# Optimization experiments

Hardware: AMD Instinct MI355X
Metric: run time of the kernel (lower is better)

## Reference

```python
import jax, jax.numpy as jnp
import numpy as np

V_W_MAX = 2.2
H = 16777216


def setup_inputs() -> dict:
    key = jax.random.key(0)
    k0, k1 = jax.random.split(key)
    x0 = jax.random.normal(k0, (4,), dtype=jnp.float32)
    U = jax.random.normal(k1, (H, 2), dtype=jnp.float32)
    dt = jnp.float32(0.05)
    return {"x0": x0, "U": U, "dt": dt}


def reference(x0, U, dt):
    # The torch loop has recurrence only in x,y (a running sum); vx,vy depend
    # solely on U[t], so the whole trajectory is elementwise + cumsum.
    vmax = jnp.float32(V_W_MAX)
    uv = jnp.tanh(U) * vmax                       # [H,2] = (vx, vy)
    pos = x0[:2] + jnp.cumsum(uv * dt, axis=0)    # [H,2] integrated x,y
    theta = jnp.arctan2(uv[:, 1], uv[:, 0] + 1e-9)            # [H]
    v = jnp.clip(jnp.sqrt(uv[:, 0] * uv[:, 0] + uv[:, 1] * uv[:, 1] + 1e-12),
                 0.0, vmax)                                    # [H]
    rest = jnp.concatenate([pos, theta[:, None], v[:, None]], axis=1)  # [H,4]
    return jnp.concatenate([x0[None, :], rest], axis=0)       # [H+1,4]
```

## Files before the change

kernel.cpp:

```cpp
#include <hip/hip_runtime.h>

#define B1 256
#define IT1 8
#define CH1 (B1 * IT1)
#define B3 256
#define IT3 8
#define CH3 (B3 * IT3)
#define B2 1024
#define VMAX 2.2f

typedef float f32x4 __attribute__((ext_vector_type(4)));

struct DSum { double x, y; };

__device__ __forceinline__ float fast_tanh(float x) {
  float e = __expf(2.0f * x);
  return 1.0f - 2.0f / (e + 1.0f);
}

__device__ __forceinline__ float fast_atan2(float y, float x) {
  float ax = fabsf(x), ay = fabsf(y);
  float mn = fminf(ax, ay), mx = fmaxf(ax, ay);
  float a = mn / (mx + 1e-30f);
  float s = a * a;
  float r = ((-0.0464964749f * s + 0.15931422f) * s - 0.327622764f) * s * a + a;
  if (ay > ax) r = 1.57079637f - r;
  if (x < 0.0f) r = 3.14159274f - r;
  return copysignf(r, y);
}

__global__ __launch_bounds__(B1) void wi_partial(
    const float* __restrict__ U, const float* __restrict__ dtp,
    DSum* __restrict__ bsum, int N)
{
  const int t = threadIdx.x;
  const int lane = t & 63, wid = t >> 6;
  const long base = (long)blockIdx.x * CH1 + (long)t * IT1;
  float sx = 0.f, sy = 0.f;
  if (base + IT1 <= (long)N) {
    const f32x4* p = (const f32x4*)(U + 2 * base);
    #pragma unroll
    for (int i = 0; i < IT1 / 2; ++i) {
      f32x4 a = p[i];
      sx += fast_tanh(a.x) + fast_tanh(a.z);
      sy += fast_tanh(a.y) + fast_tanh(a.w);
    }
  } else {
    for (int i = 0; i < IT1; ++i) {
      long idx = base + i;
      if (idx < N) { sx += fast_tanh(U[2*idx]); sy += fast_tanh(U[2*idx+1]); }
    }
  }
  #pragma unroll
  for (int o = 1; o < 64; o <<= 1) { sx += __shfl_xor(sx, o); sy += __shfl_xor(sy, o); }
  __shared__ double wsx[B1/64], wsy[B1/64];
  if (lane == 0) { wsx[wid] = (double)sx; wsy[wid] = (double)sy; }
  __syncthreads();
  if (t == 0) {
    const float sc = VMAX * (*dtp);
    double ax = 0.0, ay = 0.0;
    #pragma unroll
    for (int w = 0; w < B1/64; ++w) { ax += wsx[w]; ay += wsy[w]; }
    bsum[blockIdx.x].x = ax * (double)sc;
    bsum[blockIdx.x].y = ay * (double)sc;
  }
}

__global__ __launch_bounds__(B2) void wi_scan_blocks(DSum* bsum, int nblocks)
{
  const int t = threadIdx.x;
  const int lane = t & 63, wid = t >> 6;
  const int per = (nblocks + B2 - 1) / B2;
  const int s = t * per;
  const int e = min(s + per, nblocks);
  double tx = 0.0, ty = 0.0;
  for (int i = s; i < e; ++i) { tx += bsum[i].x; ty += bsum[i].y; }
  double ix = tx, iy = ty;
  #pragma unroll
  for (int o = 1; o < 64; o <<= 1) {
    double ux = __shfl_up(ix, o);
    double uy = __shfl_up(iy, o);
    if (lane >= o) { ix += ux; iy += uy; }
  }
  __shared__ double wx[B2/64], wy[B2/64];
  if (lane == 63) { wx[wid] = ix; wy[wid] = iy; }
  __syncthreads();
  double wbx = 0.0, wby = 0.0;
  #pragma unroll
  for (int w = 0; w < B2/64; ++w) {
    if (w < wid) { wbx += wx[w]; wby += wy[w]; }
  }
  double rx = wbx + ix - tx;
  double ry = wby + iy - ty;
  for (int i = s; i < e; ++i) {
    double vx = bsum[i].x, vy = bsum[i].y;
    bsum[i].x = rx; bsum[i].y = ry;
    rx += vx; ry += vy;
  }
}

__global__ __launch_bounds__(B3) void wi_emit(
    const float* __restrict__ U, const float* __restrict__ x0,
    const float* __restrict__ dtp, const DSum* __restrict__ boff,
    float* __restrict__ out, int N)
{
  __shared__ f32x4 stage[CH3];
  __shared__ float wsum_x[B3/64], wsum_y[B3/64];

  const int t = threadIdx.x;
  const int lane = t & 63, wid = t >> 6;
  const long base = (long)blockIdx.x * CH3 + (long)t * IT3;
  const float dt = *dtp;

  float vx[IT3], vy[IT3];
  const bool full = (base + IT3 <= (long)N);
  if (full) {
    const f32x4* p = (const f32x4*)(U + 2 * base);
    #pragma unroll
    for (int i = 0; i < IT3 / 2; ++i) {
      f32x4 a = p[i];
      vx[2*i]   = fast_tanh(a.x) * VMAX; vy[2*i]   = fast_tanh(a.y) * VMAX;
      vx[2*i+1] = fast_tanh(a.z) * VMAX; vy[2*i+1] = fast_tanh(a.w) * VMAX;
    }
  } else {
    for (int i = 0; i < IT3; ++i) {
      long idx = base + i;
      if (idx < N) { vx[i] = fast_tanh(U[2*idx]) * VMAX; vy[i] = fast_tanh(U[2*idx+1]) * VMAX; }
      else { vx[i] = 0.f; vy[i] = 0.f; }
    }
  }

  float px[IT3], py[IT3];
  float sx = 0.f, sy = 0.f;
  #pragma unroll
  for (int i = 0; i < IT3; ++i) { sx += vx[i]*dt; px[i] = sx; sy += vy[i]*dt; py[i] = sy; }
  const float totx = sx, toty = sy;

  #pragma unroll
  for (int o = 1; o < 64; o <<= 1) {
    float ux = __shfl_up(sx, o);
    float uy = __shfl_up(sy, o);
    if (lane >= o) { sx += ux; sy += uy; }
  }
  if (lane == 63) { wsum_x[wid] = sx; wsum_y[wid] = sy; }
  __syncthreads();
  float wbx = 0.f, wby = 0.f;
  #pragma unroll
  for (int w = 0; w < B3/64; ++w) {
    if (w < wid) { wbx += wsum_x[w]; wby += wsum_y[w]; }
  }
  const float exb = wbx + sx - totx;
  const float eyb = wby + sy - toty;

  const double ox = boff[blockIdx.x].x + (double)x0[0];
  const double oy = boff[blockIdx.x].y + (double)x0[1];

  #pragma unroll
  for (int i = 0; i < IT3; ++i) {
    float posx = (float)(ox + (double)(exb + px[i]));
    float posy = (float)(oy + (double)(eyb + py[i]));
    float th = fast_atan2(vy[i], vx[i] + 1e-9f);
    float vv = fminf(sqrtf(vx[i]*vx[i] + vy[i]*vy[i] + 1e-12f), VMAX);
    f32x4 r; r.x = posx; r.y = posy; r.z = th; r.w = vv;
    const int k = t * IT3 + i;
    stage[k ^ ((k >> 3) & 7)] = r;
  }
  __syncthreads();

  const long tile0 = (long)blockIdx.x * CH3;
  f32x4* o4 = (f32x4*)out;
  #pragma unroll
  for (int i = 0; i < IT3; ++i) {
    const int k = i * B3 + t;
    const long g = tile0 + k;
    if (g < (long)N) __builtin_nontemporal_store(stage[k ^ ((k >> 3) & 7)], o4 + 1 + g);
  }
  if (blockIdx.x == 0 && t == 0) {
    f32x4 r; r.x = x0[0]; r.y = x0[1]; r.z = x0[2]; r.w = x0[3];
    o4[0] = r;
  }
}

extern "C" void kernel_launch(void* const* d_in, const int* in_sizes, int n_in,
                              void* d_out, int out_size, void* d_ws, size_t ws_size,
                              hipStream_t stream) {
  const float* x0 = (const float*)d_in[0];
  const float* U  = (const float*)d_in[1];
  const float* dt = (const float*)d_in[2];
  float* out = (float*)d_out;
  const int N = in_sizes[1] / 2;
  const int nb1 = (N + CH1 - 1) / CH1;
  const int nb3 = (N + CH3 - 1) / CH3;
  DSum* bsum = (DSum*)d_ws;

  wi_partial<<<nb1, B1, 0, stream>>>(U, dt, bsum, N);
  wi_scan_blocks<<<1, B2, 0, stream>>>(bsum, nb1);
  wi_emit<<<nb3, B3, 0, stream>>>(U, x0, dt, bsum, out, N);
}
```

Measured before the change: 108.5 us.

## Use strided element mapping in emit kernel to drop LDS staging transpose

The emit kernel now assigns elements to threads with stride B3, so loads and output stores are directly coalesced. The shared-memory staging buffer and the per-thread serial prefix are gone. In their place, each of the 8 rows gets its own wave-level shuffle scan, combined through small per-row shared arrays. This removes the LDS round trip and one barrier, but costs 8 times more shuffle-scan work and narrower 8-byte loads.

```diff
diff --git a/kernel.cpp b/kernel.cpp
--- a/kernel.cpp
+++ b/kernel.cpp
@@ -10,6 +10,7 @@
 #define VMAX 2.2f
 
 typedef float f32x4 __attribute__((ext_vector_type(4)));
+typedef float f32x2 __attribute__((ext_vector_type(2)));
 
 struct DSum { double x, y; };
 
@@ -104,80 +105,74 @@
     const float* __restrict__ dtp, const DSum* __restrict__ boff,
     float* __restrict__ out, int N)
 {
-  __shared__ f32x4 stage[CH3];
-  __shared__ float wsum_x[B3/64], wsum_y[B3/64];
-
   const int t = threadIdx.x;
   const int lane = t & 63, wid = t >> 6;
-  const long base = (long)blockIdx.x * CH3 + (long)t * IT3;
+  const long tile0 = (long)blockIdx.x * CH3;
   const float dt = *dtp;
 
-  float vx[IT3], vy[IT3];
-  const bool full = (base + IT3 <= (long)N);
-  if (full) {
-    const f32x4* p = (const f32x4*)(U + 2 * base);
+  float uvx[IT3], uvy[IT3];
+  #pragma unroll
+  for (int r = 0; r < IT3; ++r) {
+    const long idx = tile0 + (long)r * B3 + t;
+    f32x2 a;
+    if (idx < (long)N) a = *(const f32x2*)(U + 2 * idx);
+    else { a.x = 0.f; a.y = 0.f; }
+    uvx[r] = fast_tanh(a.x) * VMAX;
+    uvy[r] = fast_tanh(a.y) * VMAX;
+  }
+
+  float isx[IT3], isy[IT3];
+  #pragma unroll
+  for (int r = 0; r < IT3; ++r) { isx[r] = uvx[r] * dt; isy[r] = uvy[r] * dt; }
+  #pragma unroll
+  for (int o = 1; o < 64; o <<= 1) {
     #pragma unroll
-    for (int i = 0; i < IT3 / 2; ++i) {
-      f32x4 a = p[i];
-      vx[2*i]   = fast_tanh(a.x) * VMAX; vy[2*i]   = fast_tanh(a.y) * VMAX;
-      vx[2*i+1] = fast_tanh(a.z) * VMAX; vy[2*i+1] = fast_tanh(a.w) * VMAX;
-    }
-  } else {
-    for (int i = 0; i < IT3; ++i) {
-      long idx = base + i;
-      if (idx < N) { vx[i] = fast_tanh(U[2*idx]) * VMAX; vy[i] = fast_tanh(U[2*idx+1]) * VMAX; }
-      else { vx[i] = 0.f; vy[i] = 0.f; }
+    for (int r = 0; r < IT3; ++r) {
+      float ux = __shfl_up(isx[r], o);
+      float uy = __shfl_up(isy[r], o);
+      if (lane >= o) { isx[r] += ux; isy[r] += uy; }
     }
   }
 
-  float px[IT3], py[IT3];
-  float sx = 0.f, sy = 0.f;
+  __shared__ float wtx[IT3][B3/64], wty[IT3][B3/64];
+  if (lane == 63) {
+    #pragma unroll
+    for (int r = 0; r < IT3; ++r) { wtx[r][wid] = isx[r]; wty[r][wid] = isy[r]; }
+  }
+  __syncthreads();
+  float offx[IT3], offy[IT3];
+  float rax = 0.f, ray = 0.f;
   #pragma unroll
-  for (int i = 0; i < IT3; ++i) { sx += vx[i]*dt; px[i] = sx; sy += vy[i]*dt; py[i] = sy; }
-  const float totx = sx, toty = sy;
-
-  #pragma unroll
-  for (int o = 1; o < 64; o <<= 1) {
-    float ux = __shfl_up(sx, o);
-    float uy = __shfl_up(sy, o);
-    if (lane >= o) { sx += ux; sy += uy; }
+  for (int r = 0; r < IT3; ++r) {
+    float wox = 0.f, woy = 0.f, rtx = 0.f, rty = 0.f;
+    #pragma unroll
+    for (int w = 0; w < B3/64; ++w) {
+      float a = wtx[r][w], b = wty[r][w];
+      if (w < wid) { wox += a; woy += b; }
+      rtx += a; rty += b;
+    }
+    offx[r] = rax + wox; offy[r] = ray + woy;
+    rax += rtx; ray += rty;
   }
-  if (lane == 63) { wsum_x[wid] = sx; wsum_y[wid] = sy; }
-  __syncthreads();
-  float wbx = 0.f, wby = 0.f;
-  #pragma unroll
-  for (int w = 0; w < B3/64; ++w) {
-    if (w < wid) { wbx += wsum_x[w]; wby += wsum_y[w]; }
-  }
-  const float exb = wbx + sx - totx;
-  const float eyb = wby + sy - toty;
 
   const double ox = boff[blockIdx.x].x + (double)x0[0];
   const double oy = boff[blockIdx.x].y + (double)x0[1];
-
-  #pragma unroll
-  for (int i = 0; i < IT3; ++i) {
-    float posx = (float)(ox + (double)(exb + px[i]));
-    float posy = (float)(oy + (double)(eyb + py[i]));
-    float th = fast_atan2(vy[i], vx[i] + 1e-9f);
-    float vv = fminf(sqrtf(vx[i]*vx[i] + vy[i]*vy[i] + 1e-12f), VMAX);
-    f32x4 r; r.x = posx; r.y = posy; r.z = th; r.w = vv;
-    const int k = t * IT3 + i;
-    stage[k ^ ((k >> 3) & 7)] = r;
-  }
-  __syncthreads();
-
-  const long tile0 = (long)blockIdx.x * CH3;
   f32x4* o4 = (f32x4*)out;
   #pragma unroll
-  for (int i = 0; i < IT3; ++i) {
-    const int k = i * B3 + t;
-    const long g = tile0 + k;
-    if (g < (long)N) __builtin_nontemporal_store(stage[k ^ ((k >> 3) & 7)], o4 + 1 + g);
+  for (int r = 0; r < IT3; ++r) {
+    const long idx = tile0 + (long)r * B3 + t;
+    if (idx < (long)N) {
+      float posx = (float)(ox + (double)(offx[r] + isx[r]));
+      float posy = (float)(oy + (double)(offy[r] + isy[r]));
+      float th = fast_atan2(uvy[r], uvx[r] + 1e-9f);
+      float vv = fminf(sqrtf(uvx[r]*uvx[r] + uvy[r]*uvy[r] + 1e-12f), VMAX);
+      f32x4 rr; rr.x = posx; rr.y = posy; rr.z = th; rr.w = vv;
+      __builtin_nontemporal_store(rr, o4 + 1 + idx);
+    }
   }
   if (blockIdx.x == 0 && t == 0) {
-    f32x4 r; r.x = x0[0]; r.y = x0[1]; r.z = x0[2]; r.w = x0[3];
-    o4[0] = r;
+    f32x4 rr; rr.x = x0[0]; rr.y = x0[1]; rr.z = x0[2]; rr.w = x0[3];
+    o4[0] = rr;
   }
 }
 
```

Result: slower. 113.1 us (+4.2%).

## Cache tanh velocities as fp16 in workspace to halve second-pass input reads

Applied to the files above, without the earlier changes.

The first pass now computes tanh*VMAX once, packs (vx,vy) into half2 and writes it to workspace. The block sums are built from the rounded values. The emit pass then reads 4 bytes per step instead of re-reading 8 bytes of U and recomputing tanh. This cuts second-pass input traffic and recompute, but adds a 64MB write in the first pass and makes velocity, theta and v fp16-quantized, which risks tolerance failures. If the workspace is too small, it falls back to the old path.

```diff
diff --git a/kernel.cpp b/kernel.cpp
--- a/kernel.cpp
+++ b/kernel.cpp
@@ -1,15 +1,14 @@
 #include <hip/hip_runtime.h>
+#include <hip/hip_fp16.h>
 
 #define B1 256
 #define IT1 8
 #define CH1 (B1 * IT1)
-#define B3 256
-#define IT3 8
-#define CH3 (B3 * IT3)
 #define B2 1024
 #define VMAX 2.2f
 
 typedef float f32x4 __attribute__((ext_vector_type(4)));
+typedef unsigned u32x4 __attribute__((ext_vector_type(4)));
 
 struct DSum { double x, y; };
 
@@ -29,9 +28,18 @@
   return copysignf(r, y);
 }
 
-__global__ __launch_bounds__(B1) void wi_partial(
+__device__ __forceinline__ unsigned packh2(float x, float y) {
+  __half2 h = __floats2half2_rn(x, y);
+  return *(unsigned*)&h;
+}
+__device__ __forceinline__ float2 unpackh2(unsigned u) {
+  __half2 h = *(__half2*)&u;
+  return __half22float2(h);
+}
+
+__global__ __launch_bounds__(B1) void wi_prep(
     const float* __restrict__ U, const float* __restrict__ dtp,
-    DSum* __restrict__ bsum, int N)
+    unsigned* __restrict__ uvh, DSum* __restrict__ bsum, int N)
 {
   const int t = threadIdx.x;
   const int lane = t & 63, wid = t >> 6;
@@ -39,16 +47,29 @@
   float sx = 0.f, sy = 0.f;
   if (base + IT1 <= (long)N) {
     const f32x4* p = (const f32x4*)(U + 2 * base);
+    unsigned pk[IT1];
     #pragma unroll
     for (int i = 0; i < IT1 / 2; ++i) {
       f32x4 a = p[i];
-      sx += fast_tanh(a.x) + fast_tanh(a.z);
-      sy += fast_tanh(a.y) + fast_tanh(a.w);
-    }
+      unsigned q0 = packh2(fast_tanh(a.x) * VMAX, fast_tanh(a.y) * VMAX);
+      unsigned q1 = packh2(fast_tanh(a.z) * VMAX, fast_tanh(a.w) * VMAX);
+      pk[2*i] = q0; pk[2*i+1] = q1;
+      float2 r0 = unpackh2(q0), r1 = unpackh2(q1);
+      sx += r0.x + r1.x; sy += r0.y + r1.y;
+    }
+    u32x4 v0 = { pk[0], pk[1], pk[2], pk[3] };
+    u32x4 v1 = { pk[4], pk[5], pk[6], pk[7] };
+    *(u32x4*)(uvh + base) = v0;
+    *(u32x4*)(uvh + base + 4) = v1;
   } else {
     for (int i = 0; i < IT1; ++i) {
       long idx = base + i;
-      if (idx < N) { sx += fast_tanh(U[2*idx]); sy += fast_tanh(U[2*idx+1]); }
+      if (idx < N) {
+        unsigned q = packh2(fast_tanh(U[2*idx]) * VMAX, fast_tanh(U[2*idx+1]) * VMAX);
+        uvh[idx] = q;
+        float2 r = unpackh2(q);
+        sx += r.x; sy += r.y;
+      }
     }
   }
   #pragma unroll
@@ -57,12 +78,12 @@
   if (lane == 0) { wsx[wid] = (double)sx; wsy[wid] = (double)sy; }
   __syncthreads();
   if (t == 0) {
-    const float sc = VMAX * (*dtp);
+    const double dtd = (double)(*dtp);
     double ax = 0.0, ay = 0.0;
     #pragma unroll
     for (int w = 0; w < B1/64; ++w) { ax += wsx[w]; ay += wsy[w]; }
-    bsum[blockIdx.x].x = ax * (double)sc;
-    bsum[blockIdx.x].y = ay * (double)sc;
+    bsum[blockIdx.x].x = ax * dtd;
+    bsum[blockIdx.x].y = ay * dtd;
   }
 }
 
@@ -78,8 +99,7 @@
   double ix = tx, iy = ty;
   #pragma unroll
   for (int o = 1; o < 64; o <<= 1) {
-    double ux = __shfl_up(ix, o);
-    double uy = __shfl_up(iy, o);
+    double ux = __shfl_up(ix, o), uy = __shfl_up(iy, o);
     if (lane >= o) { ix += ux; iy += uy; }
   }
   __shared__ double wx[B2/64], wy[B2/64];
@@ -99,54 +119,54 @@
   }
 }
 
-__global__ __launch_bounds__(B3) void wi_emit(
-    const float* __restrict__ U, const float* __restrict__ x0,
+__global__ __launch_bounds__(B1) void wi_emit_h(
+    const unsigned* __restrict__ uvh, const float* __restrict__ x0,
     const float* __restrict__ dtp, const DSum* __restrict__ boff,
     float* __restrict__ out, int N)
 {
-  __shared__ f32x4 stage[CH3];
-  __shared__ float wsum_x[B3/64], wsum_y[B3/64];
-
-  const int t = threadIdx.x;
-  const int lane = t & 63, wid = t >> 6;
-  const long base = (long)blockIdx.x * CH3 + (long)t * IT3;
+  __shared__ f32x4 stage[CH1];
+  __shared__ float wsum_x[B1/64], wsum_y[B1/64];
+
+  const int t = threadIdx.x;
+  const int lane = t & 63, wid = t >> 6;
+  const long base = (long)blockIdx.x * CH1 + (long)t * IT1;
   const float dt = *dtp;
 
-  float vx[IT3], vy[IT3];
-  const bool full = (base + IT3 <= (long)N);
+  float vx[IT1], vy[IT1];
+  const bool full = (base + IT1 <= (long)N);
   if (full) {
-    const f32x4* p = (const f32x4*)(U + 2 * base);
-    #pragma unroll
-    for (int i = 0; i < IT3 / 2; ++i) {
-      f32x4 a = p[i];
-      vx[2*i]   = fast_tanh(a.x) * VMAX; vy[2*i]   = fast_tanh(a.y) * VMAX;
-      vx[2*i+1] = fast_tanh(a.z) * VMAX; vy[2*i+1] = fast_tanh(a.w) * VMAX;
-    }
-  } else {
-    for (int i = 0; i < IT3; ++i) {
+    u32x4 v0 = *(const u32x4*)(uvh + base);
+    u32x4 v1 = *(const u32x4*)(uvh + base + 4);
+    unsigned pk[IT1] = { v0.x, v0.y, v0.z, v0.w, v1.x, v1.y, v1.z, v1.w };
+    #pragma unroll
+    for (int i = 0; i < IT1; ++i) {
+      float2 r = unpackh2(pk[i]);
+      vx[i] = r.x; vy[i] = r.y;
+    }
+  } else {
+    for (int i = 0; i < IT1; ++i) {
       long idx = base + i;
-      if (idx < N) { vx[i] = fast_tanh(U[2*idx]) * VMAX; vy[i] = fast_tanh(U[2*idx+1]) * VMAX; }
+      if (idx < N) { float2 r = unpackh2(uvh[idx]); vx[i] = r.x; vy[i] = r.y; }
       else { vx[i] = 0.f; vy[i] = 0.f; }
     }
   }
 
-  float px[IT3], py[IT3];
+  float px[IT1], py[IT1];
   float sx = 0.f, sy = 0.f;
   #pragma unroll
-  for (int i = 0; i < IT3; ++i) { sx += vx[i]*dt; px[i] = sx; sy += vy[i]*dt; py[i] = sy; }
+  for (int i = 0; i < IT1; ++i) { sx += vx[i]*dt; px[i] = sx; sy += vy[i]*dt; py[i] = sy; }
   const float totx = sx, toty = sy;
 
   #pragma unroll
   for (int o = 1; o < 64; o <<= 1) {
-    float ux = __shfl_up(sx, o);
-    float uy = __shfl_up(sy, o);
+    float ux = __shfl_up(sx, o), uy = __shfl_up(sy, o);
     if (lane >= o) { sx += ux; sy += uy; }
   }
   if (lane == 63) { wsum_x[wid] = sx; wsum_y[wid] = sy; }
   __syncthreads();
   float wbx = 0.f, wby = 0.f;
   #pragma unroll
-  for (int w = 0; w < B3/64; ++w) {
+  for (int w = 0; w < B1/64; ++w) {
     if (w < wid) { wbx += wsum_x[w]; wby += wsum_y[w]; }
   }
   const float exb = wbx + sx - totx;
@@ -156,22 +176,133 @@
   const double oy = boff[blockIdx.x].y + (double)x0[1];
 
   #pragma unroll
-  for (int i = 0; i < IT3; ++i) {
+  for (int i = 0; i < IT1; ++i) {
     float posx = (float)(ox + (double)(exb + px[i]));
     float posy = (float)(oy + (double)(eyb + py[i]));
     float th = fast_atan2(vy[i], vx[i] + 1e-9f);
     float vv = fminf(sqrtf(vx[i]*vx[i] + vy[i]*vy[i] + 1e-12f), VMAX);
     f32x4 r; r.x = posx; r.y = posy; r.z = th; r.w = vv;
-    const int k = t * IT3 + i;
+    const int k = t * IT1 + i;
     stage[k ^ ((k >> 3) & 7)] = r;
   }
   __syncthreads();
 
-  const long tile0 = (long)blockIdx.x * CH3;
+  const long tile0 = (long)blockIdx.x * CH1;
   f32x4* o4 = (f32x4*)out;
   #pragma unroll
-  for (int i = 0; i < IT3; ++i) {
-    const int k = i * B3 + t;
+  for (int i = 0; i < IT1; ++i) {
+    const int k = i * B1 + t;
+    const long g = tile0 + k;
+    if (g < (long)N) __builtin_nontemporal_store(stage[k ^ ((k >> 3) & 7)], o4 + 1 + g);
+  }
+  if (blockIdx.x == 0 && t == 0) {
+    f32x4 r; r.x = x0[0]; r.y = x0[1]; r.z = x0[2]; r.w = x0[3];
+    o4[0] = r;
+  }
+}
+
+__global__ __launch_bounds__(B1) void wi_partial(
+    const float* __restrict__ U, const float* __restrict__ dtp,
+    DSum* __restrict__ bsum, int N)
+{
+  const int t = threadIdx.x;
+  const int lane = t & 63, wid = t >> 6;
+  const long base = (long)blockIdx.x * CH1 + (long)t * IT1;
+  float sx = 0.f, sy = 0.f;
+  if (base + IT1 <= (long)N) {
+    const f32x4* p = (const f32x4*)(U + 2 * base);
+    #pragma unroll
+    for (int i = 0; i < IT1 / 2; ++i) {
+      f32x4 a = p[i];
+      sx += fast_tanh(a.x) + fast_tanh(a.z);
+      sy += fast_tanh(a.y) + fast_tanh(a.w);
+    }
+  } else {
+    for (int i = 0; i < IT1; ++i) {
+      long idx = base + i;
+      if (idx < N) { sx += fast_tanh(U[2*idx]); sy += fast_tanh(U[2*idx+1]); }
+    }
+  }
+  #pragma unroll
+  for (int o = 1; o < 64; o <<= 1) { sx += __shfl_xor(sx, o); sy += __shfl_xor(sy, o); }
+  __shared__ double wsx[B1/64], wsy[B1/64];
+  if (lane == 0) { wsx[wid] = (double)sx; wsy[wid] = (double)sy; }
+  __syncthreads();
+  if (t == 0) {
+    const float sc = VMAX * (*dtp);
+    double ax = 0.0, ay = 0.0;
+    #pragma unroll
+    for (int w = 0; w < B1/64; ++w) { ax += wsx[w]; ay += wsy[w]; }
+    bsum[blockIdx.x].x = ax * (double)sc;
+    bsum[blockIdx.x].y = ay * (double)sc;
+  }
+}
+
+__global__ __launch_bounds__(B1) void wi_emit(
+    const float* __restrict__ U, const float* __restrict__ x0,
+    const float* __restrict__ dtp, const DSum* __restrict__ boff,
+    float* __restrict__ out, int N)
+{
+  __shared__ f32x4 stage[CH1];
+  __shared__ float wsum_x[B1/64], wsum_y[B1/64];
+  const int t = threadIdx.x;
+  const int lane = t & 63, wid = t >> 6;
+  const long base = (long)blockIdx.x * CH1 + (long)t * IT1;
+  const float dt = *dtp;
+  float vx[IT1], vy[IT1];
+  const bool full = (base + IT1 <= (long)N);
+  if (full) {
+    const f32x4* p = (const f32x4*)(U + 2 * base);
+    #pragma unroll
+    for (int i = 0; i < IT1 / 2; ++i) {
+      f32x4 a = p[i];
+      vx[2*i]   = fast_tanh(a.x) * VMAX; vy[2*i]   = fast_tanh(a.y) * VMAX;
+      vx[2*i+1] = fast_tanh(a.z) * VMAX; vy[2*i+1] = fast_tanh(a.w) * VMAX;
+    }
+  } else {
+    for (int i = 0; i < IT1; ++i) {
+      long idx = base + i;
+      if (idx < N) { vx[i] = fast_tanh(U[2*idx]) * VMAX; vy[i] = fast_tanh(U[2*idx+1]) * VMAX; }
+      else { vx[i] = 0.f; vy[i] = 0.f; }
+    }
+  }
+  float px[IT1], py[IT1];
+  float sx = 0.f, sy = 0.f;
+  #pragma unroll
+  for (int i = 0; i < IT1; ++i) { sx += vx[i]*dt; px[i] = sx; sy += vy[i]*dt; py[i] = sy; }
+  const float totx = sx, toty = sy;
+  #pragma unroll
+  for (int o = 1; o < 64; o <<= 1) {
+    float ux = __shfl_up(sx, o), uy = __shfl_up(sy, o);
+    if (lane >= o) { sx += ux; sy += uy; }
+  }
+  if (lane == 63) { wsum_x[wid] = sx; wsum_y[wid] = sy; }
+  __syncthreads();
+  float wbx = 0.f, wby = 0.f;
+  #pragma unroll
+  for (int w = 0; w < B1/64; ++w) {
+    if (w < wid) { wbx += wsum_x[w]; wby += wsum_y[w]; }
+  }
+  const float exb = wbx + sx - totx;
+  const float eyb = wby + sy - toty;
+  const double ox = boff[blockIdx.x].x + (double)x0[0];
+  const double oy = boff[blockIdx.x].y + (double)x0[1];
+  #pragma unroll
+  for (int i = 0; i < IT1; ++i) {
+    float posx = (float)(ox + (double)(exb + px[i]));
+    float posy = (float)(oy + (double)(eyb + py[i]));
+    float th = fast_atan2(vy[i], vx[i] + 1e-9f);
+    float vv = fminf(sqrtf(vx[i]*vx[i] + vy[i]*vy[i] + 1e-12f), VMAX);
+    f32x4 r; r.x = posx; r.y = posy; r.z = th; r.w = vv;
+    const int k = t * IT1 + i;
+    stage[k ^ ((k >> 3) & 7)] = r;
+  }
+  __syncthreads();
+  const long tile0 = (long)blockIdx.x * CH1;
+  f32x4* o4 = (f32x4*)out;
+  #pragma unroll
+  for (int i = 0; i < IT1; ++i) {
+    const int k = i * B1 + t;
     const long g = tile0 + k;
     if (g < (long)N) __builtin_nontemporal_store(stage[k ^ ((k >> 3) & 7)], o4 + 1 + g);
   }
@@ -189,11 +320,21 @@
   const float* dt = (const float*)d_in[2];
   float* out = (float*)d_out;
   const int N = in_sizes[1] / 2;
-  const int nb1 = (N + CH1 - 1) / CH1;
-  const int nb3 = (N + CH3 - 1) / CH3;
-  DSum* bsum = (DSum*)d_ws;
-
-  wi_partial<<<nb1, B1, 0, stream>>>(U, dt, bsum, N);
-  wi_scan_blocks<<<1, B2, 0, stream>>>(bsum, nb1);
-  wi_emit<<<nb3, B3, 0, stream>>>(U, x0, dt, bsum, out, N);
-}
+  const int nb = (N + CH1 - 1) / CH1;
+
+  const size_t uvh_bytes = ((size_t)N * 4 + 255) & ~(size_t)255;
+  const size_t needed = uvh_bytes + (size_t)nb * sizeof(DSum);
+
+  if (ws_size >= needed) {
+    unsigned* uvh = (unsigned*)d_ws;
+    DSum* bsum = (DSum*)((char*)d_ws + uvh_bytes);
+    wi_prep<<<nb, B1, 0, stream>>>(U, dt, uvh, bsum, N);
+    wi_scan_blocks<<<1, B2, 0, stream>>>(bsum, nb);
+    wi_emit_h<<<nb, B1, 0, stream>>>(uvh, x0, dt, bsum, out, N);
+  } else {
+    DSum* bsum = (DSum*)d_ws;
+    wi_partial<<<nb, B1, 0, stream>>>(U, dt, bsum, N);
+    wi_scan_blocks<<<1, B2, 0, stream>>>(bsum, nb);
+    wi_emit<<<nb, B1, 0, stream>>>(U, x0, dt, bsum, out, N);
+  }
+}
```

After: 114.0 us. 5.0% more time.
